# Optimization experiments

Hardware: AMD Instinct MI355X
Metric: run time of the kernel (lower is better)

The kernel has to match this reference:

```python
import jax, jax.numpy as jnp
import numpy as np

B, T, I, H, O = 128, 1024, 64, 512, 64
NOISE_STD = 0.05
DT = 0.5
G = 0.9


def setup_inputs() -> dict:
    key = jax.random.key(0)
    k_in, k_wi, k_wrec, k_wo, k_noise = jax.random.split(key, 5)
    inp = jax.random.normal(k_in, (B, T, I), dtype=jnp.float32)
    wi = jax.random.normal(k_wi, (I, H), dtype=jnp.float32)  # std=1 init
    wrec = jax.random.normal(k_wrec, (H, H), dtype=jnp.float32) * (G / np.sqrt(H))
    wo = jax.random.normal(k_wo, (H, O), dtype=jnp.float32) * (1.0 / H)
    brec = jnp.zeros((H,), dtype=jnp.float32)
    h0 = jnp.zeros((H,), dtype=jnp.float32)
    noise = jax.random.normal(k_noise, (B, T, H), dtype=jnp.float32)
    return {"input": inp, "wi": wi, "wrec": wrec, "wo": wo,
            "brec": brec, "h0": h0, "noise": noise}


def reference(input, wi, wrec, wo, brec, h0, noise):
    dt = jnp.float32(DT)
    noise_scale = jnp.float32(np.sqrt(DT) * NOISE_STD)
    # Precompute input projection + bias for all timesteps: [B,T,H]
    xw = jnp.einsum('bti,ih->bth', input, wi) + brec
    h_init = jnp.broadcast_to(h0, (input.shape[0], h0.shape[0]))

    def step(h, inputs_t):
        xw_t, n_t = inputs_t  # [B,H] each
        rec = jnp.tanh(h) @ wrec.T + xw_t
        h_new = (1.0 - dt) * h + dt * rec + noise_scale * n_t
        out_t = jnp.tanh(h_new) @ wo  # readout nonlinearity defaults to tanh
        return h_new, out_t

    # scan over time: move T to leading axis
    _, outs = jax.lax.scan(step, h_init,
                           (jnp.swapaxes(xw, 0, 1), jnp.swapaxes(noise, 0, 1)))
    return jnp.swapaxes(outs, 0, 1)  # [B,T,O]
```

## Files before the change

kernel.cpp:

```cpp
#include <hip/hip_runtime.h>


#define TSTEPS 1024
#define HDIM   512
#define IDIM   64
#define ODIM   64
#define NSCALE 0.035355339059327376f
#define SENTI  ((int)0x7F7F7F7F)

typedef short bf16x8  __attribute__((ext_vector_type(8)));
typedef float f32x4   __attribute__((ext_vector_type(4)));
typedef int   int4v   __attribute__((ext_vector_type(4)));
typedef int   int2v   __attribute__((ext_vector_type(2)));

__device__ __forceinline__ unsigned short f2bf(float f){
  unsigned u = __float_as_uint(f);
  u = (u + 0x7fffu + ((u >> 16) & 1u)) >> 16;
  return (unsigned short)u;
}
__device__ __forceinline__ float tanh_fast(float x){
  float e = __expf(2.0f * x);
  return 1.0f - 2.0f / (e + 1.0f);
}
__device__ __forceinline__ void g_store8(void* p, int2v v){
  asm volatile("global_store_dwordx2 %0, %1, off sc0 sc1" :: "v"(p), "v"(v) : "memory");
}

__global__ void prep_kernel(const float* __restrict__ wi, const float* __restrict__ wrec,
                            const float* __restrict__ wo,
                            unsigned short* __restrict__ wrecb,
                            unsigned short* __restrict__ wiT,
                            unsigned short* __restrict__ woT){
  int i = blockIdx.x * 256 + threadIdx.x;
  if (i < HDIM*HDIM){
    wrecb[i] = f2bf(wrec[i]);
  } else if (i < HDIM*HDIM + HDIM*IDIM){
    int q = i - HDIM*HDIM; int j = q >> 6, ii = q & 63;
    wiT[q] = f2bf(wi[ii*HDIM + j]);
  } else if (i < HDIM*HDIM + HDIM*IDIM + ODIM*HDIM){
    int q = i - HDIM*HDIM - HDIM*IDIM; int o = q >> 9, k = q & 511;
    woT[q] = f2bf(wo[k*ODIM + o]);
  }
}

__global__ __launch_bounds__(384, 1) void rnn_scan(
    const float* __restrict__ input, const float* __restrict__ noise,
    const float* __restrict__ brec,  const float* __restrict__ h0,
    const unsigned short* __restrict__ wrecb,
    const unsigned short* __restrict__ wiT,
    const unsigned short* __restrict__ woT,
    unsigned short* __restrict__ tanhbuf,
    float* __restrict__ out)
{
  __shared__ __align__(16) short lds_tanh[32768];
  __shared__ volatile int mbox[2];

  const int tid = threadIdx.x, bid = blockIdx.x;
  const int g = bid & 7, s = bid >> 3;
  const int l = tid & 63, w = tid >> 6;
  const bool ro_on = (s < 4);
  const int TL = ro_on ? TSTEPS : TSTEPS - 1;
  char* const tbb = (char*)tanhbuf;

  if (tid == 0){ mbox[0] = 0; mbox[1] = 0; }
  __syncthreads();

  if (w < 4){
    const int lr = l & 15, kg = l >> 4, b0 = g * 16;
    const int jrow = s*64 + w*16 + lr;

    bf16x8 Arec[16];
#pragma unroll
    for (int kt = 0; kt < 16; ++kt)
      Arec[kt] = *(const bf16x8*)(wrecb + jrow*HDIM + kt*32 + kg*8);
    bf16x8 Awi0 = *(const bf16x8*)(wiT + jrow*IDIM +  0 + kg*8);
    bf16x8 Awi1 = *(const bf16x8*)(wiT + jrow*IDIM + 32 + kg*8);
    bf16x8 Awo[16] = {};
    if (ro_on){
      const int ocol = s*16 + lr;
#pragma unroll
      for (int ci = 0; ci < 16; ++ci)
        Awo[ci] = *(const bf16x8*)(woT + ocol*HDIM + ci*32 + kg*8);
    }

    const int j0 = s*64 + w*16 + 4*kg;
    const f32x4 brec4 = *(const f32x4*)(brec + j0);
    const f32x4 h04   = *(const f32x4*)(h0 + j0);
    float h[4] = {h04[0], h04[1], h04[2], h04[3]};
    const float* nbase = noise + ((long)(b0 + lr))*TSTEPS*HDIM + j0;
    const float* irow  = input + ((long)(b0 + lr))*TSTEPS*IDIM;
    const int pub_off = s*2048 + (w>>1)*1024
                      + (lr + 16*((w&1)*2 + (kg>>1)))*16 + (kg&1)*8;
    const f32x4 zero4 = {0.f, 0.f, 0.f, 0.f};

    auto pack8 = [&](float4 a, float4 b) -> bf16x8 {
      bf16x8 r;
      r[0]=(short)f2bf(a.x); r[1]=(short)f2bf(a.y); r[2]=(short)f2bf(a.z); r[3]=(short)f2bf(a.w);
      r[4]=(short)f2bf(b.x); r[5]=(short)f2bf(b.y); r[6]=(short)f2bf(b.z); r[7]=(short)f2bf(b.w);
      return r;
    };

    {
      int2v pv;
      pv.x = (int)((unsigned)f2bf(tanh_fast(h04[0])) | ((unsigned)f2bf(tanh_fast(h04[1])) << 16));
      pv.y = (int)((unsigned)f2bf(tanh_fast(h04[2])) | ((unsigned)f2bf(tanh_fast(h04[3])) << 16));
      g_store8(tbb + g*16384 + pub_off, pv);
    }
    f32x4 nz4 = *(const f32x4*)nbase;
    f32x4 acc_xw;
    {
      const float* ip = irow;
      float4 fa = *(const float4*)(ip + 8*kg),      fb = *(const float4*)(ip + 8*kg + 4);
      float4 fc = *(const float4*)(ip + 32 + 8*kg), fd = *(const float4*)(ip + 32 + 8*kg + 4);
      acc_xw = __builtin_amdgcn_mfma_f32_16x16x32_bf16(Awi0, pack8(fa,fb), zero4, 0,0,0);
      acc_xw = __builtin_amdgcn_mfma_f32_16x16x32_bf16(Awi1, pack8(fc,fd), acc_xw, 0,0,0);
    }

    for (int t = 0; t <= TL; ++t){
      const bool comp = (t < TSTEPS);
      float4 fA{}, fB{}, fC{}, fD{}; f32x4 nzn = zero4;
      if (t + 1 < TSTEPS){
        const float* ip = irow + (t + 1)*IDIM;
        fA = *(const float4*)(ip + 8*kg);      fB = *(const float4*)(ip + 8*kg + 4);
        fC = *(const float4*)(ip + 32 + 8*kg); fD = *(const float4*)(ip + 32 + 8*kg + 4);
        nzn = *(const f32x4*)(nbase + (long)(t + 1)*HDIM);
      }
      __builtin_amdgcn_sched_barrier(0);
      asm volatile("s_waitcnt vmcnt(0)" ::: "memory");
      while (mbox[0] < t + 1 || mbox[1] < t + 1) {}
      if (t >= 1 && comp){
        int2v sv; sv.x = SENTI; sv.y = SENTI;
        g_store8(tbb + (((t+3)&3)*8 + g)*16384 + pub_off, sv);
      }
      bf16x8 q[16];
      const char* lb = (const char*)lds_tanh + (t&3)*16384 + l*16;
#pragma unroll
      for (int kt = 0; kt < 16; ++kt) q[kt] = *(const bf16x8*)(lb + kt*1024);
      if (comp){
        f32x4 ac[4] = {acc_xw, zero4, zero4, zero4};
#pragma unroll
        for (int kt = 0; kt < 16; ++kt)
          ac[kt & 3] = __builtin_amdgcn_mfma_f32_16x16x32_bf16(Arec[kt], q[kt], ac[kt & 3], 0, 0, 0);
        float tb[4];
#pragma unroll
        for (int r = 0; r < 4; ++r){
          float rec = ac[0][r] + ac[1][r] + ac[2][r] + ac[3][r] + brec4[r];
          float hn  = 0.5f*h[r] + 0.5f*rec + NSCALE*nz4[r];
          h[r] = hn;
          tb[r] = tanh_fast(hn);
        }
        int2v pv;
        pv.x = (int)((unsigned)f2bf(tb[0]) | ((unsigned)f2bf(tb[1]) << 16));
        pv.y = (int)((unsigned)f2bf(tb[2]) | ((unsigned)f2bf(tb[3]) << 16));
        g_store8(tbb + (((t+1)&3)*8 + g)*16384 + pub_off, pv);
        if (t + 1 < TSTEPS) nz4 = nzn;
      }
      if (t >= 1 && ro_on){
        f32x4 ro = zero4;
#pragma unroll
        for (int ci = 0; ci < 16; ++ci)
          ro = __builtin_amdgcn_mfma_f32_16x16x32_bf16(Awo[ci], q[ci], ro, 0, 0, 0);
        if ((lr >> 2) == w)
          *(f32x4*)(out + (((long)(b0 + lr))*TSTEPS + (t - 1))*ODIM + s*16 + 4*kg) = ro;
      }
      if (t + 1 < TSTEPS){
        acc_xw = __builtin_amdgcn_mfma_f32_16x16x32_bf16(Awi0, pack8(fA,fB), zero4, 0,0,0);
        acc_xw = __builtin_amdgcn_mfma_f32_16x16x32_bf16(Awi1, pack8(fC,fD), acc_xw, 0,0,0);
      }
    }
  } else {
    const int pw = w - 4;
    for (int u = 0; u <= TL; ++u){
      const char* sb0 = tbb + ((u&3)*8 + g)*16384 + pw*8192 + l*16;
      const char* sb1 = sb0 + 4096;
      char*       lb  = (char*)lds_tanh + (u&3)*16384 + pw*8192 + l*16;
      int4v c0, c1, c2, c3, c4, c5, c6, c7;
#define PISS(CV, B, IMM) \
      asm volatile("global_load_dwordx4 %0, %1, off offset:" #IMM " sc0 sc1" \
                   : "=v"(CV) : "v"(B) : "memory")
      PISS(c0,sb0,0); PISS(c1,sb0,1024); PISS(c2,sb0,2048); PISS(c3,sb0,3072);
      PISS(c4,sb1,0); PISS(c5,sb1,1024); PISS(c6,sb1,2048); PISS(c7,sb1,3072);
      unsigned pend = 0xFFu;
      for (;;){
        asm volatile("s_waitcnt vmcnt(0)" ::: "memory");
        __builtin_amdgcn_sched_barrier(0);
        unsigned np = 0;
#define PCH(J, CV) if (pend & (1u<<J)){ \
          int bad = (CV[0]==SENTI)|(CV[1]==SENTI)|(CV[2]==SENTI)|(CV[3]==SENTI); \
          if (__any(bad)) np |= (1u<<J); else *(int4v*)(lb + J*1024) = CV; }
        PCH(0,c0) PCH(1,c1) PCH(2,c2) PCH(3,c3)
        PCH(4,c4) PCH(5,c5) PCH(6,c6) PCH(7,c7)
#undef PCH
        if (!np) break;
#define PRL(J, CV, B, IMM) if (np & (1u<<J)) PISS(CV, B, IMM);
        PRL(0,c0,sb0,0) PRL(1,c1,sb0,1024) PRL(2,c2,sb0,2048) PRL(3,c3,sb0,3072)
        PRL(4,c4,sb1,0) PRL(5,c5,sb1,1024) PRL(6,c6,sb1,2048) PRL(7,c7,sb1,3072)
#undef PRL
        pend = np;
      }
#undef PISS
      asm volatile("s_waitcnt lgkmcnt(0)" ::: "memory");
      if (l == 0) mbox[pw] = u + 1;
    }
  }
}

extern "C" void kernel_launch(void* const* d_in, const int* in_sizes, int n_in,
                              void* d_out, int out_size, void* d_ws, size_t ws_size,
                              hipStream_t stream){
  (void)in_sizes; (void)n_in; (void)ws_size; (void)out_size;
  const float* input = (const float*)d_in[0];
  const float* wi    = (const float*)d_in[1];
  const float* wrec  = (const float*)d_in[2];
  const float* wo    = (const float*)d_in[3];
  const float* brec  = (const float*)d_in[4];
  const float* h0    = (const float*)d_in[5];
  const float* noise = (const float*)d_in[6];
  float* out = (float*)d_out;

  char* ws = (char*)d_ws;
  unsigned short* wrecb = (unsigned short*)(ws);
  unsigned short* wiT   = (unsigned short*)(ws + 524288);
  unsigned short* woT   = (unsigned short*)(ws + 589824);
  unsigned short* tanhb = (unsigned short*)(ws + 655360);

  hipMemsetAsync(ws + 655360, 0x7F, 524288, stream);
  prep_kernel<<<1280, 256, 0, stream>>>(wi, wrec, wo, wrecb, wiT, woT);
  rnn_scan<<<64, 384, 0, stream>>>(input, noise, brec, h0, wrecb, wiT, woT, tanhb, out);
}
```

Before: 3.043 ms.

## Probe cache coherence at runtime and use relaxed exchange stores with one poller wave

A runtime probe checks whether blocks of the same batch group can see each other's plain stores under sc0 loads. If they can, the tanh exchange switches from system-coherent (sc0 sc1) stores and loads to cheaper plain stores and sc0 loads. The two poller waves are merged into one that loads all 16 chunks, cutting the block to 320 threads and a single mailbox. The step loop is also restructured to double-buffer the input and noise prefetch and to interleave the readout MFMAs with the recurrent ones. The probe assumes same-group blocks share an L2, which may not hold on a multi-XCD chip, so it adds a startup cost and the fallback path.

```diff
diff --git a/kernel.cpp b/kernel.cpp
--- a/kernel.cpp
+++ b/kernel.cpp
@@ -13,6 +13,9 @@
 typedef int   int4v   __attribute__((ext_vector_type(4)));
 typedef int   int2v   __attribute__((ext_vector_type(2)));
 
+template<bool B> struct BC { static constexpr bool v = B; };
+template<int I>  struct IC { static constexpr int  v = I; };
+
 __device__ __forceinline__ unsigned short f2bf(float f){
   unsigned u = __float_as_uint(f);
   u = (u + 0x7fffu + ((u >> 16) & 1u)) >> 16;
@@ -22,8 +25,30 @@
   float e = __expf(2.0f * x);
   return 1.0f - 2.0f / (e + 1.0f);
 }
-__device__ __forceinline__ void g_store8(void* p, int2v v){
-  asm volatile("global_store_dwordx2 %0, %1, off sc0 sc1" :: "v"(p), "v"(v) : "memory");
+template<bool FAST>
+__device__ __forceinline__ void ex_store8(void* p, int2v v){
+  if constexpr (FAST)
+    asm volatile("global_store_dwordx2 %0, %1, off" :: "v"(p), "v"(v) : "memory");
+  else
+    asm volatile("global_store_dwordx2 %0, %1, off sc0 sc1" :: "v"(p), "v"(v) : "memory");
+}
+__device__ __forceinline__ void st_plain4(unsigned* p, unsigned v){
+  asm volatile("global_store_dword %0, %1, off" :: "v"(p), "v"(v) : "memory");
+}
+__device__ __forceinline__ void st_llc4(unsigned* p, unsigned v){
+  asm volatile("global_store_dword %0, %1, off sc0 sc1" :: "v"(p), "v"(v) : "memory");
+}
+__device__ __forceinline__ unsigned ld_sc0(const unsigned* p){
+  unsigned r;
+  asm volatile("global_load_dword %0, %1, off sc0\n\ts_waitcnt vmcnt(0)"
+               : "=v"(r) : "v"(p) : "memory");
+  return r;
+}
+__device__ __forceinline__ unsigned ld_llc(const unsigned* p){
+  unsigned r;
+  asm volatile("global_load_dword %0, %1, off sc0 sc1\n\ts_waitcnt vmcnt(0)"
+               : "=v"(r) : "v"(p) : "memory");
+  return r;
 }
 
 __global__ void prep_kernel(const float* __restrict__ wi, const float* __restrict__ wrec,
@@ -43,166 +68,209 @@
   }
 }
 
-__global__ __launch_bounds__(384, 1) void rnn_scan(
+__global__ __launch_bounds__(320, 1) void rnn_scan(
     const float* __restrict__ input, const float* __restrict__ noise,
     const float* __restrict__ brec,  const float* __restrict__ h0,
     const unsigned short* __restrict__ wrecb,
     const unsigned short* __restrict__ wiT,
     const unsigned short* __restrict__ woT,
     unsigned short* __restrict__ tanhbuf,
+    unsigned int*  __restrict__ probe,
+    unsigned int*  __restrict__ verdict,
     float* __restrict__ out)
 {
   __shared__ __align__(16) short lds_tanh[32768];
-  __shared__ volatile int mbox[2];
+  __shared__ int mbox0;
+  __shared__ int fast_s;
 
   const int tid = threadIdx.x, bid = blockIdx.x;
   const int g = bid & 7, s = bid >> 3;
   const int l = tid & 63, w = tid >> 6;
+  const int lr = l & 15, kg = l >> 4, b0 = g * 16;
   const bool ro_on = (s < 4);
   const int TL = ro_on ? TSTEPS : TSTEPS - 1;
   char* const tbb = (char*)tanhbuf;
-
-  if (tid == 0){ mbox[0] = 0; mbox[1] = 0; }
-  __syncthreads();
-
+  const f32x4 zero4 = {0.f, 0.f, 0.f, 0.f};
+
+  if (tid == 0){ mbox0 = 0; fast_s = 0; }
+
+  const int jrow = s*64 + w*16 + lr;
+  bf16x8 Arec[16]; bf16x8 Awi0{}, Awi1{}; bf16x8 Awo[16] = {};
+  const int j0 = s*64 + w*16 + 4*kg;
+  f32x4 brec4 = zero4; float h[4] = {0.f,0.f,0.f,0.f};
+  const float* nbase = noise + ((long)(b0 + lr))*TSTEPS*HDIM + j0;
+  const float* irow  = input + ((long)(b0 + lr))*TSTEPS*IDIM;
+  const int pub_off = s*2048 + (w>>1)*1024
+                    + (lr + 16*((w&1)*2 + (kg>>1)))*16 + (kg&1)*8;
   if (w < 4){
-    const int lr = l & 15, kg = l >> 4, b0 = g * 16;
-    const int jrow = s*64 + w*16 + lr;
-
-    bf16x8 Arec[16];
 #pragma unroll
     for (int kt = 0; kt < 16; ++kt)
       Arec[kt] = *(const bf16x8*)(wrecb + jrow*HDIM + kt*32 + kg*8);
-    bf16x8 Awi0 = *(const bf16x8*)(wiT + jrow*IDIM +  0 + kg*8);
-    bf16x8 Awi1 = *(const bf16x8*)(wiT + jrow*IDIM + 32 + kg*8);
-    bf16x8 Awo[16] = {};
+    Awi0 = *(const bf16x8*)(wiT + jrow*IDIM +  0 + kg*8);
+    Awi1 = *(const bf16x8*)(wiT + jrow*IDIM + 32 + kg*8);
     if (ro_on){
       const int ocol = s*16 + lr;
 #pragma unroll
       for (int ci = 0; ci < 16; ++ci)
         Awo[ci] = *(const bf16x8*)(woT + ocol*HDIM + ci*32 + kg*8);
     }
-
-    const int j0 = s*64 + w*16 + 4*kg;
-    const f32x4 brec4 = *(const f32x4*)(brec + j0);
-    const f32x4 h04   = *(const f32x4*)(h0 + j0);
-    float h[4] = {h04[0], h04[1], h04[2], h04[3]};
-    const float* nbase = noise + ((long)(b0 + lr))*TSTEPS*HDIM + j0;
-    const float* irow  = input + ((long)(b0 + lr))*TSTEPS*IDIM;
-    const int pub_off = s*2048 + (w>>1)*1024
-                      + (lr + 16*((w&1)*2 + (kg>>1)))*16 + (kg&1)*8;
-    const f32x4 zero4 = {0.f, 0.f, 0.f, 0.f};
-
-    auto pack8 = [&](float4 a, float4 b) -> bf16x8 {
-      bf16x8 r;
-      r[0]=(short)f2bf(a.x); r[1]=(short)f2bf(a.y); r[2]=(short)f2bf(a.z); r[3]=(short)f2bf(a.w);
-      r[4]=(short)f2bf(b.x); r[5]=(short)f2bf(b.y); r[6]=(short)f2bf(b.z); r[7]=(short)f2bf(b.w);
-      return r;
-    };
-
-    {
-      int2v pv;
-      pv.x = (int)((unsigned)f2bf(tanh_fast(h04[0])) | ((unsigned)f2bf(tanh_fast(h04[1])) << 16));
-      pv.y = (int)((unsigned)f2bf(tanh_fast(h04[2])) | ((unsigned)f2bf(tanh_fast(h04[3])) << 16));
-      g_store8(tbb + g*16384 + pub_off, pv);
+    brec4 = *(const f32x4*)(brec + j0);
+    f32x4 h04 = *(const f32x4*)(h0 + j0);
+#pragma unroll
+    for (int r = 0; r < 4; ++r) h[r] = h04[r];
+  }
+
+  if (w == 0){
+    if (l == 0) st_plain4(probe + bid*16, 1u);
+    unsigned ok = 1;
+    if (l < 8){
+      const unsigned* pp = probe + (g + 8*l)*16;
+      int seen = 0;
+      for (int it = 0; it < 600 && !seen; ++it) seen = (ld_sc0(pp) != 0);
+      ok = (unsigned)seen;
     }
-    f32x4 nz4 = *(const f32x4*)nbase;
-    f32x4 acc_xw;
-    {
-      const float* ip = irow;
-      float4 fa = *(const float4*)(ip + 8*kg),      fb = *(const float4*)(ip + 8*kg + 4);
-      float4 fc = *(const float4*)(ip + 32 + 8*kg), fd = *(const float4*)(ip + 32 + 8*kg + 4);
-      acc_xw = __builtin_amdgcn_mfma_f32_16x16x32_bf16(Awi0, pack8(fa,fb), zero4, 0,0,0);
-      acc_xw = __builtin_amdgcn_mfma_f32_16x16x32_bf16(Awi1, pack8(fc,fd), acc_xw, 0,0,0);
+    ok = __all((l < 8) ? (int)ok : 1) ? 1u : 0u;
+    if (l == 0) st_llc4(verdict + bid*16, ok + 1u);
+    unsigned af = 1;
+    if (l < 8){
+      const unsigned* vp = verdict + (g + 8*l)*16;
+      unsigned v; do { v = ld_llc(vp); } while (v == 0);
+      af = (v == 2u);
     }
-
-    for (int t = 0; t <= TL; ++t){
-      const bool comp = (t < TSTEPS);
-      float4 fA{}, fB{}, fC{}, fD{}; f32x4 nzn = zero4;
-      if (t + 1 < TSTEPS){
-        const float* ip = irow + (t + 1)*IDIM;
-        fA = *(const float4*)(ip + 8*kg);      fB = *(const float4*)(ip + 8*kg + 4);
-        fC = *(const float4*)(ip + 32 + 8*kg); fD = *(const float4*)(ip + 32 + 8*kg + 4);
-        nzn = *(const f32x4*)(nbase + (long)(t + 1)*HDIM);
+    af = __all((l < 8) ? (int)af : 1) ? 1u : 0u;
+    if (l == 0) fast_s = (int)af;
+  }
+  __syncthreads();
+  const bool FASTRUN = (fast_s != 0);
+
+  auto run = [&](auto fc){
+    constexpr bool FAST = decltype(fc)::v;
+    if (w < 4){
+      auto pack8 = [&](float4 a, float4 b) -> bf16x8 {
+        bf16x8 r;
+        r[0]=(short)f2bf(a.x); r[1]=(short)f2bf(a.y); r[2]=(short)f2bf(a.z); r[3]=(short)f2bf(a.w);
+        r[4]=(short)f2bf(b.x); r[5]=(short)f2bf(b.y); r[6]=(short)f2bf(b.z); r[7]=(short)f2bf(b.w);
+        return r;
+      };
+      {
+        int2v pv;
+        pv.x = (int)((unsigned)f2bf(tanh_fast(h[0])) | ((unsigned)f2bf(tanh_fast(h[1])) << 16));
+        pv.y = (int)((unsigned)f2bf(tanh_fast(h[2])) | ((unsigned)f2bf(tanh_fast(h[3])) << 16));
+        ex_store8<FAST>(tbb + g*16384 + pub_off, pv);
       }
-      __builtin_amdgcn_sched_barrier(0);
-      asm volatile("s_waitcnt vmcnt(0)" ::: "memory");
-      while (mbox[0] < t + 1 || mbox[1] < t + 1) {}
-      if (t >= 1 && comp){
-        int2v sv; sv.x = SENTI; sv.y = SENTI;
-        g_store8(tbb + (((t+3)&3)*8 + g)*16384 + pub_off, sv);
+      f32x4  nz[2]; float4 fi[2][4];
+      nz[0] = *(const f32x4*)nbase;
+      fi[0][0] = *(const float4*)(irow + 8*kg);
+      fi[0][1] = *(const float4*)(irow + 8*kg + 4);
+      fi[0][2] = *(const float4*)(irow + 32 + 8*kg);
+      fi[0][3] = *(const float4*)(irow + 32 + 8*kg + 4);
+      nz[1] = zero4; fi[1][0]=fi[0][0]; fi[1][1]=fi[0][1]; fi[1][2]=fi[0][2]; fi[1][3]=fi[0][3];
+
+      auto step = [&](int t, auto pc){
+        constexpr int P = decltype(pc)::v;
+        const bool comp = (t < TSTEPS);
+        asm volatile("s_waitcnt vmcnt(0)" ::: "memory");
+        while (*(volatile int*)&mbox0 < t + 1) {}
+        __builtin_amdgcn_sched_barrier(0);
+        if (t + 1 < TSTEPS){
+          const float* ip = irow + (t + 1)*IDIM;
+          fi[1-P][0] = *(const float4*)(ip + 8*kg);
+          fi[1-P][1] = *(const float4*)(ip + 8*kg + 4);
+          fi[1-P][2] = *(const float4*)(ip + 32 + 8*kg);
+          fi[1-P][3] = *(const float4*)(ip + 32 + 8*kg + 4);
+          nz[1-P]    = *(const f32x4*)(nbase + (long)(t + 1)*HDIM);
+        }
+        if (t >= 1 && comp){
+          int2v sv; sv.x = SENTI; sv.y = SENTI;
+          ex_store8<FAST>(tbb + (((t + 3)&3)*8 + g)*16384 + pub_off, sv);
+        }
+        f32x4 ac0 = zero4, ac1 = zero4, ac2 = zero4, ac3 = zero4, ro = zero4;
+        if (comp){
+          ac0 = __builtin_amdgcn_mfma_f32_16x16x32_bf16(Awi0, pack8(fi[P][0], fi[P][1]), zero4, 0,0,0);
+          ac0 = __builtin_amdgcn_mfma_f32_16x16x32_bf16(Awi1, pack8(fi[P][2], fi[P][3]), ac0, 0,0,0);
+        }
+        const bool rdo = (t >= 1) && ro_on;
+        const char* lb = (const char*)lds_tanh + (t&3)*16384 + l*16;
+#pragma unroll
+        for (int kt = 0; kt < 16; ++kt){
+          bf16x8 qk = *(const bf16x8*)(lb + kt*1024);
+          if (comp){
+            if      ((kt&3)==0) ac0 = __builtin_amdgcn_mfma_f32_16x16x32_bf16(Arec[kt], qk, ac0, 0,0,0);
+            else if ((kt&3)==1) ac1 = __builtin_amdgcn_mfma_f32_16x16x32_bf16(Arec[kt], qk, ac1, 0,0,0);
+            else if ((kt&3)==2) ac2 = __builtin_amdgcn_mfma_f32_16x16x32_bf16(Arec[kt], qk, ac2, 0,0,0);
+            else                ac3 = __builtin_amdgcn_mfma_f32_16x16x32_bf16(Arec[kt], qk, ac3, 0,0,0);
+          }
+          if (rdo) ro = __builtin_amdgcn_mfma_f32_16x16x32_bf16(Awo[kt], qk, ro, 0,0,0);
+        }
+        if (comp){
+          float tb[4];
+#pragma unroll
+          for (int r = 0; r < 4; ++r){
+            float rec = ac0[r] + ac1[r] + ac2[r] + ac3[r] + brec4[r];
+            float hn  = 0.5f*h[r] + 0.5f*rec + NSCALE*nz[P][r];
+            h[r] = hn;
+            tb[r] = tanh_fast(hn);
+          }
+          int2v pv;
+          pv.x = (int)((unsigned)f2bf(tb[0]) | ((unsigned)f2bf(tb[1]) << 16));
+          pv.y = (int)((unsigned)f2bf(tb[2]) | ((unsigned)f2bf(tb[3]) << 16));
+          ex_store8<FAST>(tbb + (((t + 1)&3)*8 + g)*16384 + pub_off, pv);
+        }
+        if (rdo && (lr >> 2) == w)
+          *(f32x4*)(out + (((long)(b0 + lr))*TSTEPS + (t - 1))*ODIM + s*16 + 4*kg) = ro;
+      };
+
+      for (int t = 0; t <= TL; t += 2){
+        step(t, IC<0>{});
+        if (t + 1 <= TL) step(t + 1, IC<1>{});
       }
-      bf16x8 q[16];
-      const char* lb = (const char*)lds_tanh + (t&3)*16384 + l*16;
-#pragma unroll
-      for (int kt = 0; kt < 16; ++kt) q[kt] = *(const bf16x8*)(lb + kt*1024);
-      if (comp){
-        f32x4 ac[4] = {acc_xw, zero4, zero4, zero4};
-#pragma unroll
-        for (int kt = 0; kt < 16; ++kt)
-          ac[kt & 3] = __builtin_amdgcn_mfma_f32_16x16x32_bf16(Arec[kt], q[kt], ac[kt & 3], 0, 0, 0);
-        float tb[4];
-#pragma unroll
-        for (int r = 0; r < 4; ++r){
-          float rec = ac[0][r] + ac[1][r] + ac[2][r] + ac[3][r] + brec4[r];
-          float hn  = 0.5f*h[r] + 0.5f*rec + NSCALE*nz4[r];
-          h[r] = hn;
-          tb[r] = tanh_fast(hn);
-        }
-        int2v pv;
-        pv.x = (int)((unsigned)f2bf(tb[0]) | ((unsigned)f2bf(tb[1]) << 16));
-        pv.y = (int)((unsigned)f2bf(tb[2]) | ((unsigned)f2bf(tb[3]) << 16));
-        g_store8(tbb + (((t+1)&3)*8 + g)*16384 + pub_off, pv);
-        if (t + 1 < TSTEPS) nz4 = nzn;
-      }
-      if (t >= 1 && ro_on){
-        f32x4 ro = zero4;
-#pragma unroll
-        for (int ci = 0; ci < 16; ++ci)
-          ro = __builtin_amdgcn_mfma_f32_16x16x32_bf16(Awo[ci], q[ci], ro, 0, 0, 0);
-        if ((lr >> 2) == w)
-          *(f32x4*)(out + (((long)(b0 + lr))*TSTEPS + (t - 1))*ODIM + s*16 + 4*kg) = ro;
-      }
-      if (t + 1 < TSTEPS){
-        acc_xw = __builtin_amdgcn_mfma_f32_16x16x32_bf16(Awi0, pack8(fA,fB), zero4, 0,0,0);
-        acc_xw = __builtin_amdgcn_mfma_f32_16x16x32_bf16(Awi1, pack8(fC,fD), acc_xw, 0,0,0);
+    } else {
+      for (int u = 0; u <= TL; ++u){
+        const char* p0 = tbb + ((u&3)*8 + g)*16384 + l*16;
+        const char* p1 = p0 + 4096; const char* p2 = p0 + 8192; const char* p3 = p0 + 12288;
+        char* lb = (char*)lds_tanh + (u&3)*16384 + l*16;
+        int4v c0,c1,c2,c3,c4,c5,c6,c7,c8,c9,c10,c11,c12,c13,c14,c15;
+#define PISS(CV, B, IMM) do{ if constexpr (FAST) { \
+          asm volatile("global_load_dwordx4 %0, %1, off offset:" #IMM " sc0" \
+                       : "=v"(CV) : "v"(B) : "memory"); \
+        } else { \
+          asm volatile("global_load_dwordx4 %0, %1, off offset:" #IMM " sc0 sc1" \
+                       : "=v"(CV) : "v"(B) : "memory"); } }while(0)
+        PISS(c0,p0,0); PISS(c1,p0,1024); PISS(c2,p0,2048); PISS(c3,p0,3072);
+        PISS(c4,p1,0); PISS(c5,p1,1024); PISS(c6,p1,2048); PISS(c7,p1,3072);
+        PISS(c8,p2,0); PISS(c9,p2,1024); PISS(c10,p2,2048); PISS(c11,p2,3072);
+        PISS(c12,p3,0); PISS(c13,p3,1024); PISS(c14,p3,2048); PISS(c15,p3,3072);
+        unsigned pend = 0xFFFFu;
+        for (;;){
+          asm volatile("s_waitcnt vmcnt(0)" ::: "memory");
+          __builtin_amdgcn_sched_barrier(0);
+          unsigned np = 0;
+#define PCH(J, CV) if (pend & (1u<<J)){ \
+            int bad = (CV[0]==SENTI)|(CV[1]==SENTI)|(CV[2]==SENTI)|(CV[3]==SENTI); \
+            if (__any(bad)) np |= (1u<<J); else *(int4v*)(lb + J*1024) = CV; }
+          PCH(0,c0)  PCH(1,c1)  PCH(2,c2)  PCH(3,c3)
+          PCH(4,c4)  PCH(5,c5)  PCH(6,c6)  PCH(7,c7)
+          PCH(8,c8)  PCH(9,c9)  PCH(10,c10) PCH(11,c11)
+          PCH(12,c12) PCH(13,c13) PCH(14,c14) PCH(15,c15)
+#undef PCH
+          if (!np) break;
+#define PRL(J, CV, B, IMM) if (np & (1u<<J)) PISS(CV, B, IMM);
+          PRL(0,c0,p0,0) PRL(1,c1,p0,1024) PRL(2,c2,p0,2048) PRL(3,c3,p0,3072)
+          PRL(4,c4,p1,0) PRL(5,c5,p1,1024) PRL(6,c6,p1,2048) PRL(7,c7,p1,3072)
+          PRL(8,c8,p2,0) PRL(9,c9,p2,1024) PRL(10,c10,p2,2048) PRL(11,c11,p2,3072)
+          PRL(12,c12,p3,0) PRL(13,c13,p3,1024) PRL(14,c14,p3,2048) PRL(15,c15,p3,3072)
+#undef PRL
+          pend = np;
+        }
+#undef PISS
+        asm volatile("s_waitcnt lgkmcnt(0)" ::: "memory");
+        *(volatile int*)&mbox0 = u + 1;
       }
     }
-  } else {
-    const int pw = w - 4;
-    for (int u = 0; u <= TL; ++u){
-      const char* sb0 = tbb + ((u&3)*8 + g)*16384 + pw*8192 + l*16;
-      const char* sb1 = sb0 + 4096;
-      char*       lb  = (char*)lds_tanh + (u&3)*16384 + pw*8192 + l*16;
-      int4v c0, c1, c2, c3, c4, c5, c6, c7;
-#define PISS(CV, B, IMM) \
-      asm volatile("global_load_dwordx4 %0, %1, off offset:" #IMM " sc0 sc1" \
-                   : "=v"(CV) : "v"(B) : "memory")
-      PISS(c0,sb0,0); PISS(c1,sb0,1024); PISS(c2,sb0,2048); PISS(c3,sb0,3072);
-      PISS(c4,sb1,0); PISS(c5,sb1,1024); PISS(c6,sb1,2048); PISS(c7,sb1,3072);
-      unsigned pend = 0xFFu;
-      for (;;){
-        asm volatile("s_waitcnt vmcnt(0)" ::: "memory");
-        __builtin_amdgcn_sched_barrier(0);
-        unsigned np = 0;
-#define PCH(J, CV) if (pend & (1u<<J)){ \
-          int bad = (CV[0]==SENTI)|(CV[1]==SENTI)|(CV[2]==SENTI)|(CV[3]==SENTI); \
-          if (__any(bad)) np |= (1u<<J); else *(int4v*)(lb + J*1024) = CV; }
-        PCH(0,c0) PCH(1,c1) PCH(2,c2) PCH(3,c3)
-        PCH(4,c4) PCH(5,c5) PCH(6,c6) PCH(7,c7)
-#undef PCH
-        if (!np) break;
-#define PRL(J, CV, B, IMM) if (np & (1u<<J)) PISS(CV, B, IMM);
-        PRL(0,c0,sb0,0) PRL(1,c1,sb0,1024) PRL(2,c2,sb0,2048) PRL(3,c3,sb0,3072)
-        PRL(4,c4,sb1,0) PRL(5,c5,sb1,1024) PRL(6,c6,sb1,2048) PRL(7,c7,sb1,3072)
-#undef PRL
-        pend = np;
-      }
-#undef PISS
-      asm volatile("s_waitcnt lgkmcnt(0)" ::: "memory");
-      if (l == 0) mbox[pw] = u + 1;
-    }
-  }
+  };
+
+  if (FASTRUN) run(BC<true>{});
+  else         run(BC<false>{});
 }
 
 extern "C" void kernel_launch(void* const* d_in, const int* in_sizes, int n_in,
@@ -223,8 +291,12 @@
   unsigned short* wiT   = (unsigned short*)(ws + 524288);
   unsigned short* woT   = (unsigned short*)(ws + 589824);
   unsigned short* tanhb = (unsigned short*)(ws + 655360);
+  unsigned int*   probe = (unsigned int*)  (ws + 1179648);
+  unsigned int*   verd  = (unsigned int*)  (ws + 1183744);
 
   hipMemsetAsync(ws + 655360, 0x7F, 524288, stream);
+  hipMemsetAsync(ws + 1179648, 0, 8192, stream);
   prep_kernel<<<1280, 256, 0, stream>>>(wi, wrec, wo, wrecb, wiT, woT);
-  rnn_scan<<<64, 384, 0, stream>>>(input, noise, brec, h0, wrecb, wiT, woT, tanhb, out);
-}
+  rnn_scan<<<64, 320, 0, stream>>>(input, noise, brec, h0, wrecb, wiT, woT,
+                                   tanhb, probe, verd, out);
+}
```

New measurement: 3.820 ms. 25.5% more time.
